# Kernel optimization log

Measured on AMD Instinct MI355X. Metric: run time of the kernel, lower is better.

The kernel has to match this reference:

```python
import jax, jax.numpy as jnp
import numpy as np

N_NODES = 50000
N_EDGES = 800000
N_GRAPHS = 64
D_IN = 128
D_HID = 128
D_OUT = 32
N_LAYERS = 2


def setup_inputs() -> dict:
    key = jax.random.key(0)
    ks = jax.random.split(key, 12)
    x = jax.random.normal(ks[0], (N_NODES, D_IN), dtype=jnp.float32)
    edge_index = jax.random.randint(ks[1], (2, N_EDGES), 0, N_NODES, dtype=jnp.int64)
    batch = jnp.sort(jax.random.randint(ks[2], (N_NODES,), 0, N_GRAPHS, dtype=jnp.int64))
    s = 1.0 / np.sqrt(D_HID)
    return {
        "x": x,
        "edge_index": edge_index,
        "batch": batch,
        "conv_w_rel": jax.random.normal(ks[3], (N_LAYERS, D_IN, D_HID), dtype=jnp.float32) * s,
        "conv_b_rel": jax.random.normal(ks[4], (N_LAYERS, D_HID), dtype=jnp.float32) * s,
        "conv_w_root": jax.random.normal(ks[5], (N_LAYERS, D_IN, D_HID), dtype=jnp.float32) * s,
        "sage_w_l": jax.random.normal(ks[6], (N_LAYERS, D_HID, D_HID), dtype=jnp.float32) * s,
        "sage_b_l": jax.random.normal(ks[7], (N_LAYERS, D_HID), dtype=jnp.float32) * s,
        "sage_w_r": jax.random.normal(ks[8], (N_LAYERS, D_HID, D_HID), dtype=jnp.float32) * s,
        "fc_w": jax.random.normal(ks[9], (D_HID, D_OUT), dtype=jnp.float32) * s,
        "fc_b": jax.random.normal(ks[10], (D_OUT,), dtype=jnp.float32) * s,
    }


def reference(x, edge_index, batch, conv_w_rel, conv_b_rel, conv_w_root,
              sage_w_l, sage_b_l, sage_w_r, fc_w, fc_b):
    N = x.shape[0]
    src, dst = edge_index[0], edge_index[1]
    # StandardScaler: per-feature standardization (population std)
    mu = jnp.mean(x, axis=0)
    sd = jnp.std(x, axis=0)
    h = (x - mu) / sd
    # Stacked GraphConv layers: lin_rel(sum-aggr neighbors) + lin_root(x), then ReLU
    for l in range(conv_w_rel.shape[0]):
        agg = jax.ops.segment_sum(h[src], dst, num_segments=N)  # [N, D]
        h = jax.nn.relu(agg @ conv_w_rel[l] + conv_b_rel[l] + h @ conv_w_root[l])
    # GraphSAGE: SAGEConv layers (mean aggregation), ReLU between layers only
    deg = jax.ops.segment_sum(jnp.ones((src.shape[0],), dtype=h.dtype), dst, num_segments=N)
    deg = jnp.clip(deg, 1.0)[:, None]  # [N, 1]
    L = sage_w_l.shape[0]
    for l in range(L):
        agg = jax.ops.segment_sum(h[src], dst, num_segments=N) / deg  # mean over neighbors
        h_new = agg @ sage_w_l[l] + sage_b_l[l] + h @ sage_w_r[l]
        h = jax.nn.relu(h_new) if l < L - 1 else h_new
    # global_mean_pool over graphs
    sums = jax.ops.segment_sum(h, batch, num_segments=N_GRAPHS)  # [G, D]
    cnt = jax.ops.segment_sum(jnp.ones((N,), dtype=h.dtype), batch, num_segments=N_GRAPHS)
    pooled = sums / jnp.clip(cnt, 1.0)[:, None]
    return pooled @ fc_w + fc_b  # [G, D_OUT]
```

## Files before the change

### kernel.cpp

```cpp
#include <hip/hip_runtime.h>

#define N_NODES 50000
#define N_EDGES 800000
#define N_GRAPHS 64
#define DH 128
#define DOUT 32

typedef __attribute__((ext_vector_type(8))) short bf16x8;
typedef __attribute__((ext_vector_type(4))) float f32x4;

__device__ __forceinline__ unsigned short f2bf(float f) {
    union { float f; unsigned int u; } x;
    x.f = f;
    unsigned int u = x.u;
    u += 0x7FFFu + ((u >> 16) & 1u);
    return (unsigned short)(u >> 16);
}

#define STAT_BLKS 512
__global__ __launch_bounds__(256) void stats_kernel(const float* __restrict__ x,
                                                    float* __restrict__ partial) {
    __shared__ float4 shs[256];
    __shared__ float4 shq[256];
    const int tid = threadIdx.x;
    const int rowgrp = tid >> 5;
    const int cq = tid & 31;
    float4 s = make_float4(0.f, 0.f, 0.f, 0.f);
    float4 q = make_float4(0.f, 0.f, 0.f, 0.f);
#pragma unroll 4
    for (int r = blockIdx.x * 8 + rowgrp; r < N_NODES; r += STAT_BLKS * 8) {
        const float4 v = *reinterpret_cast<const float4*>(x + (size_t)r * DH + cq * 4);
        s.x += v.x; s.y += v.y; s.z += v.z; s.w += v.w;
        q.x = fmaf(v.x, v.x, q.x); q.y = fmaf(v.y, v.y, q.y);
        q.z = fmaf(v.z, v.z, q.z); q.w = fmaf(v.w, v.w, q.w);
    }
    shs[tid] = s; shq[tid] = q;
    __syncthreads();
    for (int off = 128; off >= 32; off >>= 1) {
        if (tid < off) {
            float4 a = shs[tid], b = shs[tid + off];
            a.x += b.x; a.y += b.y; a.z += b.z; a.w += b.w;
            shs[tid] = a;
            float4 c = shq[tid], d = shq[tid + off];
            c.x += d.x; c.y += d.y; c.z += d.z; c.w += d.w;
            shq[tid] = c;
        }
        __syncthreads();
    }
    if (tid < 32) {
        const float4 a = shs[tid];
        const float4 c = shq[tid];
        const float sv[4] = {a.x, a.y, a.z, a.w};
        const float qv[4] = {c.x, c.y, c.z, c.w};
#pragma unroll
        for (int j = 0; j < 4; ++j) {
            const int col = tid * 4 + j;
            partial[(size_t)col * STAT_BLKS + blockIdx.x] = sv[j];
            partial[(size_t)(128 + col) * STAT_BLKS + blockIdx.x] = qv[j];
        }
    }
}

__global__ __launch_bounds__(128) void finalize_stats_kernel(const float* __restrict__ partial,
                                                             float* __restrict__ stat) {
    const int c = threadIdx.x;
    const float4* ps = reinterpret_cast<const float4*>(partial + (size_t)c * STAT_BLKS);
    const float4* pq = reinterpret_cast<const float4*>(partial + (size_t)(128 + c) * STAT_BLKS);
    float s = 0.f, q = 0.f;
#pragma unroll 8
    for (int b = 0; b < STAT_BLKS / 4; ++b) {
        const float4 v = ps[b];
        s += v.x + v.y + v.z + v.w;
        const float4 w = pq[b];
        q += w.x + w.y + w.z + w.w;
    }
    const float inv_n = 1.0f / (float)N_NODES;
    const float mu = s * inv_n;
    const float var = q * inv_n - mu * mu;
    const float sd = sqrtf(fmaxf(var, 1e-20f));
    stat[256 + c] = mu;
    stat[384 + c] = 1.0f / sd;
}

__global__ void standardize_kernel(const float* __restrict__ x,
                                   const float* __restrict__ stat,
                                   unsigned short* __restrict__ h) {
    const size_t i = (size_t)blockIdx.x * blockDim.x + threadIdx.x;
    const int c4 = (int)(i & 31) << 2;
    const float4 v = reinterpret_cast<const float4*>(x)[i];
    const float4 m = *reinterpret_cast<const float4*>(stat + 256 + c4);
    const float4 is = *reinterpret_cast<const float4*>(stat + 384 + c4);
    ushort4 o;
    o.x = f2bf((v.x - m.x) * is.x);
    o.y = f2bf((v.y - m.y) * is.y);
    o.z = f2bf((v.z - m.z) * is.z);
    o.w = f2bf((v.w - m.w) * is.w);
    reinterpret_cast<ushort4*>(h)[i] = o;
}

__global__ void count_deg_kernel(const int* __restrict__ dst, int* __restrict__ deg_i) {
    int e = blockIdx.x * blockDim.x + threadIdx.x;
    if (e < N_EDGES) {
        const int d = __builtin_nontemporal_load(&dst[e]);
        atomicAdd(&deg_i[d], 1);
    }
}

#define SCAN_BLK 256
#define SCAN_NBLK ((N_NODES + SCAN_BLK - 1) / SCAN_BLK)

__global__ __launch_bounds__(SCAN_BLK) void scan_local_kernel(const int* __restrict__ deg_i,
                                                              int* __restrict__ row_ptr,
                                                              int* __restrict__ bsum) {
    __shared__ int sh[SCAN_BLK];
    const int tid = threadIdx.x;
    const int idx = blockIdx.x * SCAN_BLK + tid;
    const int v = (idx < N_NODES) ? deg_i[idx] : 0;
    sh[tid] = v;
    __syncthreads();
#pragma unroll
    for (int off = 1; off < SCAN_BLK; off <<= 1) {
        const int t = (tid >= off) ? sh[tid - off] : 0;
        __syncthreads();
        sh[tid] += t;
        __syncthreads();
    }
    if (idx < N_NODES) row_ptr[idx] = sh[tid] - v;
    if (tid == SCAN_BLK - 1) bsum[blockIdx.x] = sh[tid];
}

__global__ __launch_bounds__(SCAN_BLK) void scan_bsum_kernel(int* __restrict__ bsum) {
    __shared__ int sh[SCAN_BLK];
    const int tid = threadIdx.x;
    const int v = (tid < SCAN_NBLK) ? bsum[tid] : 0;
    sh[tid] = v;
    __syncthreads();
#pragma unroll
    for (int off = 1; off < SCAN_BLK; off <<= 1) {
        const int t = (tid >= off) ? sh[tid - off] : 0;
        __syncthreads();
        sh[tid] += t;
        __syncthreads();
    }
    if (tid < SCAN_NBLK) bsum[tid] = sh[tid] - v;
}

__global__ __launch_bounds__(SCAN_BLK) void scan_finalize_kernel(const int* __restrict__ deg_i,
                                                                 const int* __restrict__ bsum,
                                                                 int* __restrict__ row_ptr,
                                                                 int* __restrict__ cursor,
                                                                 float* __restrict__ deg_inv) {
    const int tid = threadIdx.x;
    const int idx = blockIdx.x * SCAN_BLK + tid;
    if (idx < N_NODES) {
        const int excl = row_ptr[idx] + bsum[blockIdx.x];
        row_ptr[idx] = excl;
        cursor[idx] = excl;
        const int d = deg_i[idx];
        deg_inv[idx] = 1.0f / (float)(d > 1 ? d : 1);
    }
    if (idx == 0) row_ptr[N_NODES] = N_EDGES;
}

#define NXCD 8
#define RANGE_NODES ((N_NODES + NXCD - 1) / NXCD)
#define SC_SLICES 104
__global__ __launch_bounds__(256) void scatter_ranged_kernel(const int* __restrict__ src,
                                                             const int* __restrict__ dst,
                                                             int* __restrict__ cursor,
                                                             int* __restrict__ csr_src) {
    const int range = blockIdx.x & (NXCD - 1);
    const int slice = blockIdx.x >> 3;
    const int lo = range * RANGE_NODES;
    const int hi = min(lo + RANGE_NODES, N_NODES);
    const int stride = SC_SLICES * 256;
    for (int e = slice * 256 + threadIdx.x; e < N_EDGES; e += stride) {
        const int d = __builtin_nontemporal_load(&dst[e]);
        if (d >= lo && d < hi) {
            const int s = __builtin_nontemporal_load(&src[e]);
            const int pos = atomicAdd(&cursor[d], 1);
            csr_src[pos] = s;
        }
    }
}

__global__ __launch_bounds__(256) void aggregate_csr_kernel(const unsigned short* __restrict__ h,
                                                            const int* __restrict__ row_ptr,
                                                            const int* __restrict__ csr_src,
                                                            const float* __restrict__ deg_inv,
                                                            unsigned short* __restrict__ agg,
                                                            const int useScale) {
    const int node = blockIdx.x * 4 + (threadIdx.x >> 6);
    if (node >= N_NODES) return;
    const int lane = threadIdx.x & 63;
    const int beg = row_ptr[node];
    const int end = row_ptr[node + 1];
    float a0 = 0.f, a1 = 0.f;
    for (int chunk = beg; chunk < end; chunk += 64) {
        const int cnt = min(64, end - chunk);
        const int sv = (lane < cnt) ? __builtin_nontemporal_load(&csr_src[chunk + lane]) : 0;
        int j = 0;
        for (; j + 8 <= cnt; j += 8) {
            int ss[8];
#pragma unroll
            for (int u = 0; u < 8; ++u) ss[u] = __shfl(sv, j + u);
            unsigned int vv[8];
#pragma unroll
            for (int u = 0; u < 8; ++u)
                vv[u] = *reinterpret_cast<const unsigned int*>(h + (size_t)ss[u] * DH + lane * 2);
#pragma unroll
            for (int u = 0; u < 8; ++u) {
                union { unsigned int x; float f; } t;
                t.x = vv[u] << 16; a0 += t.f;
                t.x = vv[u] & 0xFFFF0000u; a1 += t.f;
            }
        }
        for (; j < cnt; ++j) {
            const int s = __shfl(sv, j);
            const unsigned int v = *reinterpret_cast<const unsigned int*>(h + (size_t)s * DH + lane * 2);
            union { unsigned int x; float f; } t;
            t.x = v << 16; a0 += t.f;
            t.x = v & 0xFFFF0000u; a1 += t.f;
        }
    }
    float o0 = a0, o1 = a1;
    if (useScale) {
        const float sc = deg_inv[node];
        o0 *= sc; o1 *= sc;
    }
    const unsigned int packed = (unsigned int)f2bf(o0) | ((unsigned int)f2bf(o1) << 16);
    reinterpret_cast<unsigned int*>(agg + (size_t)node * DH)[lane] = packed;
}

__global__ void pack_w_kernel(const float* __restrict__ cwr, const float* __restrict__ cwroot,
                              const float* __restrict__ swl, const float* __restrict__ swr,
                              unsigned short* __restrict__ wfrag) {
    const int g = blockIdx.x * blockDim.x + threadIdx.x;
    if (g >= 16384) return;
    const int lane = g & 63;
    const int n = (g >> 6) & 7;
    const int t = (g >> 9) & 3;
    const int phase = (g >> 11) & 1;
    const int layer = (g >> 12) & 3;
    const float* W1 = (layer < 2) ? (cwr + layer * 16384) : (swl + (layer - 2) * 16384);
    const float* W2 = (layer < 2) ? (cwroot + layer * 16384) : (swr + (layer - 2) * 16384);
    const float* W = phase ? W2 : W1;
    const int col = n * 16 + (lane & 15);
    const int k0 = t * 32 + (lane >> 4) * 8;
    unsigned short v[8];
#pragma unroll
    for (int j = 0; j < 8; ++j) v[j] = f2bf(W[(size_t)(k0 + j) * DH + col]);
    unsigned short* dstp = wfrag + ((size_t)g * 8);
#pragma unroll
    for (int j = 0; j < 8; ++j) dstp[j] = v[j];
}

__global__ __launch_bounds__(256) void fused_layer_mfma_kernel(
    const unsigned short* __restrict__ A1, const unsigned short* __restrict__ A2,
    const unsigned short* __restrict__ Wf, const float* __restrict__ bias,
    unsigned short* __restrict__ Cb, float* __restrict__ Cf, const int relu) {
    const int wid = threadIdx.x >> 6;
    const int lane = threadIdx.x & 63;
    const int row0 = blockIdx.x * 64 + wid * 16;
    const int arow = row0 + (lane & 15);
    const int koff = (lane >> 4) * 8;
    const bool rowOK = (arow < N_NODES);

    f32x4 acc[8];
#pragma unroll
    for (int n = 0; n < 8; ++n) acc[n] = (f32x4){0.f, 0.f, 0.f, 0.f};

#pragma unroll
    for (int phase = 0; phase < 2; ++phase) {
        const unsigned short* Ar = (phase ? A2 : A1) + (size_t)arow * DH;
        const unsigned short* Wp = Wf + (size_t)phase * (4 * 8 * 64 * 8);
#pragma unroll
        for (int t = 0; t < 4; ++t) {
            bf16x8 af = {};
            if (rowOK) af = *reinterpret_cast<const bf16x8*>(Ar + t * 32 + koff);
            const unsigned short* wt = Wp + (((size_t)t * 8) * 64 + lane) * 8;
#pragma unroll
            for (int n = 0; n < 8; ++n) {
                const bf16x8 bfv = *reinterpret_cast<const bf16x8*>(wt + (size_t)n * 64 * 8);
                acc[n] = __builtin_amdgcn_mfma_f32_16x16x32_bf16(af, bfv, acc[n], 0, 0, 0);
            }
        }
    }

    const int crow0 = row0 + (lane >> 4) * 4;
    const int ccol = lane & 15;
#pragma unroll
    for (int n = 0; n < 8; ++n) {
        const int col = n * 16 + ccol;
        const float bv = bias[col];
#pragma unroll
        for (int r = 0; r < 4; ++r) {
            const int grow = crow0 + r;
            if (grow >= N_NODES) continue;
            float v = acc[n][r] + bv;
            if (relu) {
                v = fmaxf(v, 0.f);
                Cb[(size_t)grow * DH + col] = f2bf(v);
            } else {
                Cf[(size_t)grow * DH + col] = v;
            }
        }
    }
}

#define POOL_BLOCKS 512
__global__ __launch_bounds__(128) void pool_seg_kernel(const float* __restrict__ h,
                                                       const int* __restrict__ batch,
                                                       float* __restrict__ pooled,
                                                       float* __restrict__ cnt) {
    const int c = threadIdx.x;
    const int nper = (N_NODES + POOL_BLOCKS - 1) / POOL_BLOCKS;
    const int n0 = blockIdx.x * nper;
    const int n1 = min(n0 + nper, N_NODES);
    if (n0 >= n1) return;
    float acc = 0.f;
    int g = batch[n0];
    int runlen = 0;
    for (int n = n0; n < n1; ++n) {
        const int bg = batch[n];
        if (bg != g) {
            atomicAdd(&pooled[(size_t)g * DH + c], acc);
            if (c == 0) atomicAdd(&cnt[g], (float)runlen);
            acc = 0.f; runlen = 0; g = bg;
        }
        acc += h[(size_t)n * DH + c];
        ++runlen;
    }
    atomicAdd(&pooled[(size_t)g * DH + c], acc);
    if (c == 0) atomicAdd(&cnt[g], (float)runlen);
}

__global__ void final_kernel(const float* __restrict__ pooled, const float* __restrict__ cnt,
                             const float* __restrict__ fcw, const float* __restrict__ fcb,
                             float* __restrict__ out) {
    const int g = blockIdx.x;
    const int j = threadIdx.x;
    if (j >= DOUT) return;
    const float inv = 1.0f / fmaxf(cnt[g], 1.0f);
    float acc = fcb[j];
    for (int d = 0; d < DH; ++d)
        acc = fmaf(pooled[(size_t)g * DH + d] * inv, fcw[(size_t)d * DOUT + j], acc);
    out[(size_t)g * DOUT + j] = acc;
}

extern "C" void kernel_launch(void* const* d_in, const int* in_sizes, int n_in,
                              void* d_out, int out_size, void* d_ws, size_t ws_size,
                              hipStream_t stream) {
    const float* x = (const float*)d_in[0];
    const int* ei = (const int*)d_in[1];
    const int* batch = (const int*)d_in[2];
    const float* conv_w_rel = (const float*)d_in[3];
    const float* conv_b_rel = (const float*)d_in[4];
    const float* conv_w_root = (const float*)d_in[5];
    const float* sage_w_l = (const float*)d_in[6];
    const float* sage_b_l = (const float*)d_in[7];
    const float* sage_w_r = (const float*)d_in[8];
    const float* fc_w = (const float*)d_in[9];
    const float* fc_b = (const float*)d_in[10];
    float* out = (float*)d_out;

    const int* src = ei;
    const int* dst = ei + N_EDGES;

    const size_t NHB = (size_t)N_NODES * DH * sizeof(unsigned short);
    const size_t NFB = (size_t)N_NODES * DH * sizeof(float);
    char* p = (char*)d_ws;
    unsigned short* hb0 = (unsigned short*)p; p += NHB;
    unsigned short* hb1 = (unsigned short*)p; p += NHB;
    unsigned short* aggb = (unsigned short*)p; p += NHB;
    float* hF = (float*)p; p += NFB;
    float* deg_inv = (float*)p; p += ((size_t)N_NODES * sizeof(float) + 255) & ~(size_t)255;
    float* stat = (float*)p; p += 512 * sizeof(float);
    float* pooled = (float*)p; p += (size_t)N_GRAPHS * DH * sizeof(float);
    float* cnt = (float*)p; p += ((size_t)N_GRAPHS * sizeof(float) + 255) & ~(size_t)255;
    int* deg_i = (int*)p; p += ((size_t)N_NODES * sizeof(int) + 255) & ~(size_t)255;
    int* row_ptr = (int*)p; p += ((size_t)(N_NODES + 1) * sizeof(int) + 255) & ~(size_t)255;
    int* cursor = (int*)p; p += ((size_t)N_NODES * sizeof(int) + 255) & ~(size_t)255;
    int* bsum = (int*)p; p += ((size_t)SCAN_BLK * sizeof(int) + 255) & ~(size_t)255;
    float* partial = (float*)p; p += (size_t)256 * STAT_BLKS * sizeof(float);
    unsigned short* wfrag = (unsigned short*)p; p += (size_t)4 * 32768 * sizeof(unsigned short);
    int* csr_src = (int*)p; p += (size_t)N_EDGES * sizeof(int);

    hipLaunchKernelGGL(stats_kernel, dim3(STAT_BLKS), dim3(256), 0, stream, x, partial);
    hipLaunchKernelGGL(finalize_stats_kernel, dim3(1), dim3(DH), 0, stream, partial, stat);
    hipLaunchKernelGGL(standardize_kernel, dim3((N_NODES * DH / 4) / 256), dim3(256), 0, stream,
                       x, stat, hb0);

    hipLaunchKernelGGL(pack_w_kernel, dim3(64), dim3(256), 0, stream,
                       conv_w_rel, conv_w_root, sage_w_l, sage_w_r, wfrag);

    hipMemsetAsync(deg_i, 0, (size_t)N_NODES * sizeof(int), stream);
    hipLaunchKernelGGL(count_deg_kernel, dim3((N_EDGES + 255) / 256), dim3(256), 0, stream,
                       dst, deg_i);
    hipLaunchKernelGGL(scan_local_kernel, dim3(SCAN_NBLK), dim3(SCAN_BLK), 0, stream,
                       deg_i, row_ptr, bsum);
    hipLaunchKernelGGL(scan_bsum_kernel, dim3(1), dim3(SCAN_BLK), 0, stream, bsum);
    hipLaunchKernelGGL(scan_finalize_kernel, dim3(SCAN_NBLK), dim3(SCAN_BLK), 0, stream,
                       deg_i, bsum, row_ptr, cursor, deg_inv);
    hipLaunchKernelGGL(scatter_ranged_kernel, dim3(NXCD * SC_SLICES), dim3(256), 0, stream,
                       src, dst, cursor, csr_src);

    const float* Bs[4] = {conv_b_rel, conv_b_rel + 128, sage_b_l, sage_b_l + 128};

    unsigned short* curb = hb0;
    unsigned short* nxtb = hb1;
    const dim3 aggGrid((N_NODES + 3) / 4);
    const dim3 gemmGrid((N_NODES + 63) / 64);
    for (int l = 0; l < 4; ++l) {
        hipLaunchKernelGGL(aggregate_csr_kernel, aggGrid, dim3(256), 0, stream,
                           curb, row_ptr, csr_src, deg_inv, aggb, (l >= 2) ? 1 : 0);
        hipLaunchKernelGGL(fused_layer_mfma_kernel, gemmGrid, dim3(256), 0, stream,
                           aggb, curb, wfrag + (size_t)l * 32768, Bs[l],
                           (l < 3) ? nxtb : (unsigned short*)nullptr,
                           (l < 3) ? (float*)nullptr : hF,
                           (l < 3) ? 1 : 0);
        unsigned short* t = curb; curb = nxtb; nxtb = t;
    }

    hipMemsetAsync(pooled, 0, ((size_t)N_GRAPHS * DH + N_GRAPHS) * sizeof(float), stream);
    hipLaunchKernelGGL(pool_seg_kernel, dim3(POOL_BLOCKS), dim3(DH), 0, stream,
                       hF, batch, pooled, cnt);
    hipLaunchKernelGGL(final_kernel, dim3(N_GRAPHS), dim3(64), 0, stream,
                       pooled, cnt, fc_w, fc_b, out);
}
```

Baseline: 365.3 us.

## Pre-partition edges into per-XCD buckets before CSR scatter

Adds a two-level bucketing step: a per-block histogram of destination ranges, a single-block exclusive scan, and a partition kernel that writes edges into per-range contiguous buffers. The scatter kernel then reads only its own range's edges instead of having every range scan all 800k edges and filter. This cuts redundant edge reads in the CSR build but adds two kernels, an extra 6.4MB of edge traffic, and a serial single-block scan. It also drops the nontemporal hint on csr_src loads in aggregation.

Measured after the change: 387.5 us. 6.1% more time.

```diff
diff --git a/kernel.cpp b/kernel.cpp
--- a/kernel.cpp
+++ b/kernel.cpp
@@ -98,11 +98,75 @@
     reinterpret_cast<ushort4*>(h)[i] = o;
 }
 
-__global__ void count_deg_kernel(const int* __restrict__ dst, int* __restrict__ deg_i) {
-    int e = blockIdx.x * blockDim.x + threadIdx.x;
-    if (e < N_EDGES) {
-        const int d = __builtin_nontemporal_load(&dst[e]);
-        atomicAdd(&deg_i[d], 1);
+#define NXCD 8
+#define RANGE_NODES ((N_NODES + NXCD - 1) / NXCD)
+#define PART_EPB 1024
+#define PART_NBLK ((N_EDGES + PART_EPB - 1) / PART_EPB)
+
+__global__ __launch_bounds__(256) void count_deg_hist_kernel(const int* __restrict__ dst,
+                                                             int* __restrict__ deg_i,
+                                                             int* __restrict__ hist) {
+    __shared__ int lhist[NXCD];
+    const int tid = threadIdx.x;
+    if (tid < NXCD) lhist[tid] = 0;
+    __syncthreads();
+    const int base = blockIdx.x * PART_EPB;
+#pragma unroll
+    for (int i = 0; i < 4; ++i) {
+        const int e = base + i * 256 + tid;
+        if (e < N_EDGES) {
+            const int d = dst[e];
+            atomicAdd(&deg_i[d], 1);
+            atomicAdd(&lhist[d / RANGE_NODES], 1);
+        }
+    }
+    __syncthreads();
+    if (tid < NXCD) hist[tid * PART_NBLK + blockIdx.x] = lhist[tid];
+}
+
+__global__ __launch_bounds__(256) void scan_hist_kernel(int* __restrict__ hist) {
+    __shared__ int sh[256];
+    const int tid = threadIdx.x;
+    const int TOT = NXCD * PART_NBLK;
+    int carry = 0;
+    for (int base = 0; base < TOT; base += 256) {
+        const int idx = base + tid;
+        const int v = (idx < TOT) ? hist[idx] : 0;
+        sh[tid] = v;
+        __syncthreads();
+#pragma unroll
+        for (int off = 1; off < 256; off <<= 1) {
+            const int t = (tid >= off) ? sh[tid - off] : 0;
+            __syncthreads();
+            sh[tid] += t;
+            __syncthreads();
+        }
+        if (idx < TOT) hist[idx] = carry + sh[tid] - v;
+        carry += sh[255];
+        __syncthreads();
+    }
+}
+
+__global__ __launch_bounds__(256) void partition_kernel(const int* __restrict__ src,
+                                                        const int* __restrict__ dst,
+                                                        const int* __restrict__ hist,
+                                                        int* __restrict__ ebuf_src,
+                                                        int* __restrict__ ebuf_dst) {
+    __shared__ int lcur[NXCD];
+    const int tid = threadIdx.x;
+    if (tid < NXCD) lcur[tid] = hist[tid * PART_NBLK + blockIdx.x];
+    __syncthreads();
+    const int base = blockIdx.x * PART_EPB;
+#pragma unroll
+    for (int i = 0; i < 4; ++i) {
+        const int e = base + i * 256 + tid;
+        if (e < N_EDGES) {
+            const int d = dst[e];
+            const int s = src[e];
+            const int pos = atomicAdd(&lcur[d / RANGE_NODES], 1);
+            ebuf_src[pos] = s;
+            ebuf_dst[pos] = d;
+        }
     }
 }
 
@@ -162,25 +226,22 @@
     if (idx == 0) row_ptr[N_NODES] = N_EDGES;
 }
 
-#define NXCD 8
-#define RANGE_NODES ((N_NODES + NXCD - 1) / NXCD)
-#define SC_SLICES 104
-__global__ __launch_bounds__(256) void scatter_ranged_kernel(const int* __restrict__ src,
-                                                             const int* __restrict__ dst,
+#define SC_SLICES 64
+__global__ __launch_bounds__(256) void scatter_bucket_kernel(const int* __restrict__ ebuf_src,
+                                                             const int* __restrict__ ebuf_dst,
+                                                             const int* __restrict__ hist,
                                                              int* __restrict__ cursor,
                                                              int* __restrict__ csr_src) {
     const int range = blockIdx.x & (NXCD - 1);
     const int slice = blockIdx.x >> 3;
-    const int lo = range * RANGE_NODES;
-    const int hi = min(lo + RANGE_NODES, N_NODES);
+    const int b0 = hist[range * PART_NBLK];
+    const int b1 = (range < NXCD - 1) ? hist[(range + 1) * PART_NBLK] : N_EDGES;
     const int stride = SC_SLICES * 256;
-    for (int e = slice * 256 + threadIdx.x; e < N_EDGES; e += stride) {
-        const int d = __builtin_nontemporal_load(&dst[e]);
-        if (d >= lo && d < hi) {
-            const int s = __builtin_nontemporal_load(&src[e]);
-            const int pos = atomicAdd(&cursor[d], 1);
-            csr_src[pos] = s;
-        }
+    for (int e = b0 + slice * 256 + threadIdx.x; e < b1; e += stride) {
+        const int d = ebuf_dst[e];
+        const int s = ebuf_src[e];
+        const int pos = atomicAdd(&cursor[d], 1);
+        csr_src[pos] = s;
     }
 }
 
@@ -198,7 +259,7 @@
     float a0 = 0.f, a1 = 0.f;
     for (int chunk = beg; chunk < end; chunk += 64) {
         const int cnt = min(64, end - chunk);
-        const int sv = (lane < cnt) ? __builtin_nontemporal_load(&csr_src[chunk + lane]) : 0;
+        const int sv = (lane < cnt) ? csr_src[chunk + lane] : 0;
         int j = 0;
         for (; j + 8 <= cnt; j += 8) {
             int ss[8];
@@ -385,6 +446,9 @@
     float* partial = (float*)p; p += (size_t)256 * STAT_BLKS * sizeof(float);
     unsigned short* wfrag = (unsigned short*)p; p += (size_t)4 * 32768 * sizeof(unsigned short);
     int* csr_src = (int*)p; p += (size_t)N_EDGES * sizeof(int);
+    int* ebuf_src = (int*)p; p += (size_t)N_EDGES * sizeof(int);
+    int* ebuf_dst = (int*)p; p += (size_t)N_EDGES * sizeof(int);
+    int* hist = (int*)p; p += ((size_t)NXCD * PART_NBLK * sizeof(int) + 255) & ~(size_t)255;
 
     hipLaunchKernelGGL(stats_kernel, dim3(STAT_BLKS), dim3(256), 0, stream, x, partial);
     hipLaunchKernelGGL(finalize_stats_kernel, dim3(1), dim3(DH), 0, stream, partial, stat);
@@ -395,15 +459,18 @@
                        conv_w_rel, conv_w_root, sage_w_l, sage_w_r, wfrag);
 
     hipMemsetAsync(deg_i, 0, (size_t)N_NODES * sizeof(int), stream);
-    hipLaunchKernelGGL(count_deg_kernel, dim3((N_EDGES + 255) / 256), dim3(256), 0, stream,
-                       dst, deg_i);
+    hipLaunchKernelGGL(count_deg_hist_kernel, dim3(PART_NBLK), dim3(256), 0, stream,
+                       dst, deg_i, hist);
+    hipLaunchKernelGGL(scan_hist_kernel, dim3(1), dim3(256), 0, stream, hist);
+    hipLaunchKernelGGL(partition_kernel, dim3(PART_NBLK), dim3(256), 0, stream,
+                       src, dst, hist, ebuf_src, ebuf_dst);
     hipLaunchKernelGGL(scan_local_kernel, dim3(SCAN_NBLK), dim3(SCAN_BLK), 0, stream,
                        deg_i, row_ptr, bsum);
     hipLaunchKernelGGL(scan_bsum_kernel, dim3(1), dim3(SCAN_BLK), 0, stream, bsum);
     hipLaunchKernelGGL(scan_finalize_kernel, dim3(SCAN_NBLK), dim3(SCAN_BLK), 0, stream,
                        deg_i, bsum, row_ptr, cursor, deg_inv);
-    hipLaunchKernelGGL(scatter_ranged_kernel, dim3(NXCD * SC_SLICES), dim3(256), 0, stream,
-                       src, dst, cursor, csr_src);
+    hipLaunchKernelGGL(scatter_bucket_kernel, dim3(NXCD * SC_SLICES), dim3(256), 0, stream,
+                       ebuf_src, ebuf_dst, hist, cursor, csr_src);
 
     const float* Bs[4] = {conv_b_rel, conv_b_rel + 128, sage_b_l, sage_b_l + 128};
 
```

## Fuse neighbor aggregation into MFMA layer GEMM via shared-memory staging

Applied to the files above, without the earlier changes.

Merges the CSR gather-aggregate kernel and the dual-GEMM layer kernel into one kernel per layer. Each block aggregates 32 nodes into padded LDS rows, synchronizes, then runs bf16 MFMA on the LDS tile plus the root features, with four waves splitting rows and column halves. This removes the aggregated-feature round trip through global memory and one launch per layer. In exchange, the gather phase now runs only 8 nodes per wave serially, which lowers the parallelism available for latency hiding, and the GEMM waves idle until all aggregation in the block finishes.

New measurement: 436.4 us. +19.5%, slower.

```diff
diff --git a/kernel.cpp b/kernel.cpp
--- a/kernel.cpp
+++ b/kernel.cpp
@@ -184,54 +184,6 @@
     }
 }
 
-__global__ __launch_bounds__(256) void aggregate_csr_kernel(const unsigned short* __restrict__ h,
-                                                            const int* __restrict__ row_ptr,
-                                                            const int* __restrict__ csr_src,
-                                                            const float* __restrict__ deg_inv,
-                                                            unsigned short* __restrict__ agg,
-                                                            const int useScale) {
-    const int node = blockIdx.x * 4 + (threadIdx.x >> 6);
-    if (node >= N_NODES) return;
-    const int lane = threadIdx.x & 63;
-    const int beg = row_ptr[node];
-    const int end = row_ptr[node + 1];
-    float a0 = 0.f, a1 = 0.f;
-    for (int chunk = beg; chunk < end; chunk += 64) {
-        const int cnt = min(64, end - chunk);
-        const int sv = (lane < cnt) ? __builtin_nontemporal_load(&csr_src[chunk + lane]) : 0;
-        int j = 0;
-        for (; j + 8 <= cnt; j += 8) {
-            int ss[8];
-#pragma unroll
-            for (int u = 0; u < 8; ++u) ss[u] = __shfl(sv, j + u);
-            unsigned int vv[8];
-#pragma unroll
-            for (int u = 0; u < 8; ++u)
-                vv[u] = *reinterpret_cast<const unsigned int*>(h + (size_t)ss[u] * DH + lane * 2);
-#pragma unroll
-            for (int u = 0; u < 8; ++u) {
-                union { unsigned int x; float f; } t;
-                t.x = vv[u] << 16; a0 += t.f;
-                t.x = vv[u] & 0xFFFF0000u; a1 += t.f;
-            }
-        }
-        for (; j < cnt; ++j) {
-            const int s = __shfl(sv, j);
-            const unsigned int v = *reinterpret_cast<const unsigned int*>(h + (size_t)s * DH + lane * 2);
-            union { unsigned int x; float f; } t;
-            t.x = v << 16; a0 += t.f;
-            t.x = v & 0xFFFF0000u; a1 += t.f;
-        }
-    }
-    float o0 = a0, o1 = a1;
-    if (useScale) {
-        const float sc = deg_inv[node];
-        o0 *= sc; o1 *= sc;
-    }
-    const unsigned int packed = (unsigned int)f2bf(o0) | ((unsigned int)f2bf(o1) << 16);
-    reinterpret_cast<unsigned int*>(agg + (size_t)node * DH)[lane] = packed;
-}
-
 __global__ void pack_w_kernel(const float* __restrict__ cwr, const float* __restrict__ cwroot,
                               const float* __restrict__ swl, const float* __restrict__ swr,
                               unsigned short* __restrict__ wfrag) {
@@ -255,43 +207,106 @@
     for (int j = 0; j < 8; ++j) dstp[j] = v[j];
 }
 
-__global__ __launch_bounds__(256) void fused_layer_mfma_kernel(
-    const unsigned short* __restrict__ A1, const unsigned short* __restrict__ A2,
+#define LSTRIDE 136
+#define NPB 32
+__global__ __launch_bounds__(256) void agg_layer_kernel(
+    const unsigned short* __restrict__ h,
+    const int* __restrict__ row_ptr, const int* __restrict__ csr_src,
+    const float* __restrict__ deg_inv,
     const unsigned short* __restrict__ Wf, const float* __restrict__ bias,
-    unsigned short* __restrict__ Cb, float* __restrict__ Cf, const int relu) {
+    unsigned short* __restrict__ Cb, float* __restrict__ Cf,
+    const int relu, const int useScale) {
+    __shared__ unsigned short aggs[NPB * LSTRIDE];
     const int wid = threadIdx.x >> 6;
     const int lane = threadIdx.x & 63;
-    const int row0 = blockIdx.x * 64 + wid * 16;
-    const int arow = row0 + (lane & 15);
+    const int node0 = blockIdx.x * NPB;
+
+#pragma unroll 1
+    for (int i = 0; i < 8; ++i) {
+        const int lrow = wid * 8 + i;
+        const int node = node0 + lrow;
+        unsigned int* rowp = reinterpret_cast<unsigned int*>(&aggs[lrow * LSTRIDE]);
+        if (node < N_NODES) {
+            const int beg = row_ptr[node];
+            const int end = row_ptr[node + 1];
+            float a0 = 0.f, a1 = 0.f;
+            for (int chunk = beg; chunk < end; chunk += 64) {
+                const int cnt = min(64, end - chunk);
+                const int sv = (lane < cnt) ? __builtin_nontemporal_load(&csr_src[chunk + lane]) : 0;
+                int j = 0;
+                for (; j + 8 <= cnt; j += 8) {
+                    int ss[8];
+#pragma unroll
+                    for (int u = 0; u < 8; ++u) ss[u] = __shfl(sv, j + u);
+                    unsigned int vv[8];
+#pragma unroll
+                    for (int u = 0; u < 8; ++u)
+                        vv[u] = *reinterpret_cast<const unsigned int*>(h + (size_t)ss[u] * DH + lane * 2);
+#pragma unroll
+                    for (int u = 0; u < 8; ++u) {
+                        union { unsigned int x; float f; } t;
+                        t.x = vv[u] << 16; a0 += t.f;
+                        t.x = vv[u] & 0xFFFF0000u; a1 += t.f;
+                    }
+                }
+                for (; j < cnt; ++j) {
+                    const int s = __shfl(sv, j);
+                    const unsigned int v = *reinterpret_cast<const unsigned int*>(h + (size_t)s * DH + lane * 2);
+                    union { unsigned int x; float f; } t;
+                    t.x = v << 16; a0 += t.f;
+                    t.x = v & 0xFFFF0000u; a1 += t.f;
+                }
+            }
+            float o0 = a0, o1 = a1;
+            if (useScale) {
+                const float sc = deg_inv[node];
+                o0 *= sc; o1 *= sc;
+            }
+            rowp[lane] = (unsigned int)f2bf(o0) | ((unsigned int)f2bf(o1) << 16);
+        } else {
+            rowp[lane] = 0u;
+        }
+    }
+    __syncthreads();
+
+    const int rbase = (wid >> 1) * 16;
+    const int cbase = (wid & 1) * 4;
+    const int lrow = rbase + (lane & 15);
+    const int arow = node0 + lrow;
     const int koff = (lane >> 4) * 8;
     const bool rowOK = (arow < N_NODES);
-
-    f32x4 acc[8];
-#pragma unroll
-    for (int n = 0; n < 8; ++n) acc[n] = (f32x4){0.f, 0.f, 0.f, 0.f};
+    const unsigned short* lrp = &aggs[lrow * LSTRIDE];
+
+    f32x4 acc[4];
+#pragma unroll
+    for (int n = 0; n < 4; ++n) acc[n] = (f32x4){0.f, 0.f, 0.f, 0.f};
 
 #pragma unroll
     for (int phase = 0; phase < 2; ++phase) {
-        const unsigned short* Ar = (phase ? A2 : A1) + (size_t)arow * DH;
         const unsigned short* Wp = Wf + (size_t)phase * (4 * 8 * 64 * 8);
 #pragma unroll
         for (int t = 0; t < 4; ++t) {
-            bf16x8 af = {};
-            if (rowOK) af = *reinterpret_cast<const bf16x8*>(Ar + t * 32 + koff);
+            bf16x8 af;
+            if (phase == 0) {
+                af = *reinterpret_cast<const bf16x8*>(lrp + t * 32 + koff);
+            } else {
+                af = (bf16x8){};
+                if (rowOK) af = *reinterpret_cast<const bf16x8*>(h + (size_t)arow * DH + t * 32 + koff);
+            }
             const unsigned short* wt = Wp + (((size_t)t * 8) * 64 + lane) * 8;
 #pragma unroll
-            for (int n = 0; n < 8; ++n) {
-                const bf16x8 bfv = *reinterpret_cast<const bf16x8*>(wt + (size_t)n * 64 * 8);
+            for (int n = 0; n < 4; ++n) {
+                const bf16x8 bfv = *reinterpret_cast<const bf16x8*>(wt + (size_t)(cbase + n) * 64 * 8);
                 acc[n] = __builtin_amdgcn_mfma_f32_16x16x32_bf16(af, bfv, acc[n], 0, 0, 0);
             }
         }
     }
 
-    const int crow0 = row0 + (lane >> 4) * 4;
+    const int crow0 = node0 + rbase + (lane >> 4) * 4;
     const int ccol = lane & 15;
 #pragma unroll
-    for (int n = 0; n < 8; ++n) {
-        const int col = n * 16 + ccol;
+    for (int n = 0; n < 4; ++n) {
+        const int col = (cbase + n) * 16 + ccol;
         const float bv = bias[col];
 #pragma unroll
         for (int r = 0; r < 4; ++r) {
@@ -372,7 +387,6 @@
     char* p = (char*)d_ws;
     unsigned short* hb0 = (unsigned short*)p; p += NHB;
     unsigned short* hb1 = (unsigned short*)p; p += NHB;
-    unsigned short* aggb = (unsigned short*)p; p += NHB;
     float* hF = (float*)p; p += NFB;
     float* deg_inv = (float*)p; p += ((size_t)N_NODES * sizeof(float) + 255) & ~(size_t)255;
     float* stat = (float*)p; p += 512 * sizeof(float);
@@ -409,16 +423,14 @@
 
     unsigned short* curb = hb0;
     unsigned short* nxtb = hb1;
-    const dim3 aggGrid((N_NODES + 3) / 4);
-    const dim3 gemmGrid((N_NODES + 63) / 64);
+    const dim3 layerGrid((N_NODES + NPB - 1) / NPB);
     for (int l = 0; l < 4; ++l) {
-        hipLaunchKernelGGL(aggregate_csr_kernel, aggGrid, dim3(256), 0, stream,
-                           curb, row_ptr, csr_src, deg_inv, aggb, (l >= 2) ? 1 : 0);
-        hipLaunchKernelGGL(fused_layer_mfma_kernel, gemmGrid, dim3(256), 0, stream,
-                           aggb, curb, wfrag + (size_t)l * 32768, Bs[l],
+        hipLaunchKernelGGL(agg_layer_kernel, layerGrid, dim3(256), 0, stream,
+                           curb, row_ptr, csr_src, deg_inv,
+                           wfrag + (size_t)l * 32768, Bs[l],
                            (l < 3) ? nxtb : (unsigned short*)nullptr,
                            (l < 3) ? (float*)nullptr : hF,
-                           (l < 3) ? 1 : 0);
+                           (l < 3) ? 1 : 0, (l >= 2) ? 1 : 0);
         unsigned short* t = curb; curb = nxtb; nxtb = t;
     }
 
```
